# Kernel tuning notes

Measured on AMD Instinct MI355X. Metric: run time of the kernel, lower is better.

Reference implementation:

```python
import jax, jax.numpy as jnp
import numpy as np

B, T, D, H = 4, 2048, 1024, 16
HD = D // H  # head_dim = 64

def setup_inputs() -> dict:
    key = jax.random.key(0)
    k1, k2, k3 = jax.random.split(key, 3)
    scale_in = 1.0 / np.sqrt(D)
    return {
        "x": jax.random.normal(k1, (B, T, D), dtype=jnp.float32),
        "W_qkv": jax.random.normal(k2, (D, 3 * D), dtype=jnp.float32) * scale_in,
        "b_qkv": jnp.zeros((3 * D,), dtype=jnp.float32),
        "W_out": jax.random.normal(k3, (D, D), dtype=jnp.float32) * scale_in,
        "b_out": jnp.zeros((D,), dtype=jnp.float32),
    }

def reference(x, W_qkv, b_qkv, W_out, b_out):
    Bx, Tx, C = x.shape
    qkv = x @ W_qkv + b_qkv                      # [B,T,3D]
    q, k, v = jnp.split(qkv, 3, axis=-1)
    # [B,T,D] -> [B,H,T,hd]
    def to_heads(t):
        return t.reshape(Bx, Tx, H, HD).transpose(0, 2, 1, 3)
    q, k, v = to_heads(q), to_heads(k), to_heads(v)
    scores = jnp.einsum('bhqd,bhkd->bhqk', q, k) / np.sqrt(HD)  # [B,H,T,T]
    causal = jnp.tril(jnp.ones((Tx, Tx), dtype=bool))
    scores = jnp.where(causal, scores, -jnp.inf)
    attn = jax.nn.softmax(scores, axis=-1)       # dropout p=0 -> identity
    out = jnp.einsum('bhqk,bhkd->bhqd', attn, v)  # [B,H,T,hd]
    out = out.transpose(0, 2, 1, 3).reshape(Bx, Tx, C)
    return out @ W_out + b_out
```

## Files before the change

### kernel.cpp

```cpp
#include <hip/hip_runtime.h>
#include <hip/hip_bf16.h>

#define BB 4
#define TT 2048
#define DD 1024
#define HH 16
#define HDIM 64
#define BT (BB*TT)
#define D3 (3*DD)

typedef __attribute__((ext_vector_type(8))) short bf16x8;
typedef __attribute__((ext_vector_type(4))) float f32x4;

#if __has_builtin(__builtin_amdgcn_exp2f)
#define EXP2(x) __builtin_amdgcn_exp2f(x)
#else
#define EXP2(x) exp2f(x)
#endif

__device__ __forceinline__ ushort f2bf(float f) {
  union { float f; uint32_t u; } v; v.f = f;
  uint32_t u = v.u + 0x7FFFu + ((v.u >> 16) & 1u);
  return (ushort)(u >> 16);
}

__device__ __forceinline__ ushort f2bf_hw(float f) {
  __hip_bfloat16 h = __float2bfloat16(f);
  ushort u;
  __builtin_memcpy(&u, &h, 2);
  return u;
}

__device__ __forceinline__ float bf2f(ushort u) {
  union { uint32_t i; float f; } x; x.i = ((uint32_t)u) << 16; return x.f;
}

__device__ __forceinline__ void gload_lds16(const void* g, void* l) {
  __builtin_amdgcn_global_load_lds((const __attribute__((address_space(1))) void*)g,
                                   (__attribute__((address_space(3))) void*)l, 16, 0, 0);
}

__global__ __launch_bounds__(256)
void cvt_bf16(const float* __restrict__ in, ushort* __restrict__ out, int n4,
              uint* __restrict__ ctr) {
  if (blockIdx.x == 0 && threadIdx.x == 0) *ctr = 0u;
  int i = blockIdx.x * blockDim.x + threadIdx.x;
  int stride = gridDim.x * blockDim.x;
  for (; i < n4; i += stride) {
    float4 v = ((const float4*)in)[i];
    ushort4 o;
    o.x = f2bf(v.x); o.y = f2bf(v.y); o.z = f2bf(v.z); o.w = f2bf(v.w);
    ((ushort4*)out)[i] = o;
  }
}

__global__ __launch_bounds__(256)
void transpose_cvt(const float* __restrict__ W, ushort* __restrict__ Wt, int K, int N) {
  __shared__ ushort Tt[64][68];
  const int n0 = blockIdx.x * 64;
  const int k0 = blockIdx.y * 64;
  const int tid = threadIdx.x;
  const int r = tid >> 4;
  const int c4 = (tid & 15) * 4;
  #pragma unroll
  for (int i = 0; i < 4; ++i) {
    int row = r + i * 16;
    float4 v = *(const float4*)&W[(size_t)(k0 + row) * N + n0 + c4];
    Tt[c4 + 0][row] = f2bf(v.x);
    Tt[c4 + 1][row] = f2bf(v.y);
    Tt[c4 + 2][row] = f2bf(v.z);
    Tt[c4 + 3][row] = f2bf(v.w);
  }
  __syncthreads();
  #pragma unroll
  for (int i = 0; i < 4; ++i) {
    int row = r + i * 16;
    ushort4 tv = *(const ushort4*)&Tt[row][c4];
    *(ushort4*)&Wt[(size_t)(n0 + row) * K + k0 + c4] = tv;
  }
}

template<bool F32OUT>
__global__ __launch_bounds__(512, 2)
void gemm_8p(const ushort* __restrict__ A, const ushort* __restrict__ Bw,
             const float* __restrict__ bias, void* __restrict__ C, int N) {
  __shared__ __align__(16) short lds[2 * (128 + 256) * 64];

  const int tid = threadIdx.x;
  const int w = tid >> 6;
  const int wm = w >> 2;
  const int wn = w & 3;
  const int lane = tid & 63;
  const int li = lane & 15, g = lane >> 4;
  const int swz = (li & 7) << 4;

  const int bm = blockIdx.y * 128;
  const int bn = blockIdx.x * 256;
  const ushort* Ag = A + (size_t)bm * 1024;
  const ushort* Bg = Bw + (size_t)bn * 1024;

  const int lrow8 = lane >> 3;
  const int chsw = (lane & 7) ^ lrow8;

  f32x4 acc[4][4] = {};

#define STAGE6(t, p) do { \
  const int kk_ = (t) * 64; \
  short* Ad_ = lds + (p) * 24576; \
  short* Bd_ = Ad_ + 8192; \
  _Pragma("unroll") \
  for (int h_ = 0; h_ < 2; ++h_) { \
    const int r_ = h_ * 64 + w * 8; \
    gload_lds16(Ag + (size_t)(r_ + lrow8) * 1024 + kk_ + chsw * 8, Ad_ + r_ * 64); \
  } \
  _Pragma("unroll") \
  for (int j_ = 0; j_ < 4; ++j_) { \
    const int r_ = j_ * 64 + w * 8; \
    gload_lds16(Bg + (size_t)(r_ + lrow8) * 1024 + kk_ + chsw * 8, Bd_ + r_ * 64); \
  } \
} while (0)

  STAGE6(0, 0);
  asm volatile("s_waitcnt vmcnt(0)" ::: "memory");
  __builtin_amdgcn_sched_barrier(0);
  __builtin_amdgcn_s_barrier();

  for (int s = 0; s < 16; ++s) {
    const int cur = s & 1;
    const char* Ab = (const char*)lds + cur * 49152;
    const char* Bb = Ab + 16384;

    if (s + 1 < 16) STAGE6(s + 1, cur ^ 1);

    #pragma unroll
    for (int kh = 0; kh < 2; ++kh) {
      bf16x8 af[4], bf[4];
      #pragma unroll
      for (int mi = 0; mi < 4; ++mi)
        af[mi] = *(const bf16x8*)(Ab + (wm * 64 + mi * 16 + li) * 128 + ((kh * 64 + g * 16) ^ swz));
      #pragma unroll
      for (int ni = 0; ni < 4; ++ni)
        bf[ni] = *(const bf16x8*)(Bb + (wn * 64 + ni * 16 + li) * 128 + ((kh * 64 + g * 16) ^ swz));
      __builtin_amdgcn_s_setprio(1);
      #pragma unroll
      for (int mi = 0; mi < 4; ++mi)
        #pragma unroll
        for (int ni = 0; ni < 4; ++ni)
          acc[mi][ni] = __builtin_amdgcn_mfma_f32_16x16x32_bf16(af[mi], bf[ni], acc[mi][ni], 0, 0, 0);
      __builtin_amdgcn_s_setprio(0);
      if (kh == 0) __builtin_amdgcn_s_barrier();
    }
    asm volatile("s_waitcnt vmcnt(0)" ::: "memory");
    __builtin_amdgcn_sched_barrier(0);
    __builtin_amdgcn_s_barrier();
  }
#undef STAGE6

  #pragma unroll
  for (int ni = 0; ni < 4; ++ni) {
    int col = bn + wn * 64 + ni * 16 + li;
    float bv = bias[col];
    #pragma unroll
    for (int mi = 0; mi < 4; ++mi) {
      int row = bm + wm * 64 + mi * 16 + g * 4;
      #pragma unroll
      for (int r = 0; r < 4; ++r) {
        float v = acc[mi][ni][r] + bv;
        if (F32OUT) ((float*)C)[(size_t)(row + r) * N + col] = v;
        else        ((ushort*)C)[(size_t)(row + r) * N + col] = f2bf_hw(v);
      }
    }
  }
}

#define NITEMS 1024

__global__ __launch_bounds__(256)
void attn_mfma(const ushort* __restrict__ qkv, ushort* __restrict__ out,
               uint* __restrict__ ctr) {
  __shared__ __align__(16) short Ks[64 * 64];
  __shared__ __align__(16) short Vt[64 * 64];
  __shared__ __align__(16) short Pl[4 * 16 * 64];
  __shared__ int s_item;

  const int tid = threadIdx.x;
  const int w = tid >> 6;
  const int lane = tid & 63;
  const int li = lane & 15, g = lane >> 4;
  const int sw = (li & 7) << 4;

  char* KsB = (char*)Ks;
  char* VtB = (char*)Vt;
  char* PlB = (char*)Pl + w * 2048;

  const int krow0 = tid >> 3;
  const int kc = tid & 7;
  const int d0 = (tid >> 5) * 8;
  const int kp = tid & 31;
  const int kswz = (kc * 16) ^ ((krow0 & 7) << 4);

  for (;;) {
    if (tid == 0) s_item = (int)atomicAdd(ctr, 1u);
    __syncthreads();
    const int item = s_item;
    if (item >= NITEMS) return;

    const int qt = 15 - (item >> 6);
    const int bh = item & 63;
    const int h = bh & 15, b = bh >> 4;
    const int qg0 = qt * 128 + w * 32;

    bf16x8 qfr[2][2];
    #pragma unroll
    for (int qf = 0; qf < 2; ++qf) {
      const ushort* qrow = qkv + (size_t)(b * TT + qg0 + qf * 16 + li) * D3 + h * HDIM;
      #pragma unroll
      for (int c = 0; c < 2; ++c) {
        uint4 raw = *(const uint4*)(qrow + c * 32 + g * 8);
        const ushort* rp = (const ushort*)&raw;
        bf16x8 v;
        #pragma unroll
        for (int j = 0; j < 8; ++j)
          v[j] = (short)f2bf_hw(bf2f(rp[j]) * 0.18033688f);
        qfr[qf][c] = v;
      }
    }

    f32x4 o[4][2] = {};
    float lsum[2] = {0.f, 0.f};

    const ushort* kbase = qkv + (size_t)b * TT * D3 + DD + h * HDIM;
    const ushort* vbase = kbase + DD;

    const int nt = 2 * qt + 2;
    const int itlast = 2 * qt + (w >> 1);

    uint4 kpre0, kpre1, vpre0, vpre1;
    {
      const ushort* kg = kbase + (size_t)krow0 * D3 + kc * 8;
      kpre0 = *(const uint4*)kg;
      kpre1 = *(const uint4*)(kg + (size_t)32 * D3);
      const ushort* vg = vbase + (size_t)(2 * kp) * D3 + d0;
      vpre0 = *(const uint4*)vg;
      vpre1 = *(const uint4*)(vg + D3);
    }

    for (int it = 0; it < nt; ++it) {
      const int k0 = it * 64;
      *(uint4*)(KsB + krow0 * 128 + kswz) = kpre0;
      *(uint4*)(KsB + (krow0 + 32) * 128 + kswz) = kpre1;
      {
        const ushort* pa = (const ushort*)&vpre0;
        const ushort* pb = (const ushort*)&vpre1;
        #pragma unroll
        for (int j = 0; j < 8; ++j) {
          uint32_t pk = (uint32_t)pa[j] | ((uint32_t)pb[j] << 16);
          *(uint32_t*)(VtB + (d0 + j) * 128 + ((4 * kp) ^ (j << 4))) = pk;
        }
      }
      __syncthreads();
      if (it + 1 < nt) {
        const ushort* kg = kbase + (size_t)(k0 + 64 + krow0) * D3 + kc * 8;
        kpre0 = *(const uint4*)kg;
        kpre1 = *(const uint4*)(kg + (size_t)32 * D3);
        const ushort* vg = vbase + (size_t)(k0 + 64 + 2 * kp) * D3 + d0;
        vpre0 = *(const uint4*)vg;
        vpre1 = *(const uint4*)(vg + D3);
      }
      if (it <= itlast) {
        const bool domask = (it == itlast);
        bf16x8 pf[2][2];
        f32x4 s[2][4];
        __builtin_amdgcn_s_setprio(1);
        #pragma unroll
        for (int kt = 0; kt < 4; ++kt) {
          const int row = kt * 16 + li;
          bf16x8 kf0 = *(bf16x8*)(KsB + row * 128 + ((g * 16) ^ sw));
          bf16x8 kf1 = *(bf16x8*)(KsB + row * 128 + ((64 + g * 16) ^ sw));
          #pragma unroll
          for (int qf = 0; qf < 2; ++qf) {
            f32x4 a = {0.f, 0.f, 0.f, 0.f};
            a = __builtin_amdgcn_mfma_f32_16x16x32_bf16(kf0, qfr[qf][0], a, 0, 0, 0);
            a = __builtin_amdgcn_mfma_f32_16x16x32_bf16(kf1, qfr[qf][1], a, 0, 0, 0);
            s[qf][kt] = a;
          }
        }
        __builtin_amdgcn_s_setprio(0);
        #pragma unroll
        for (int qf = 0; qf < 2; ++qf) {
          const int qrow = qg0 + qf * 16 + li;
          if (domask) {
            #pragma unroll
            for (int kt = 0; kt < 4; ++kt)
              #pragma unroll
              for (int r = 0; r < 4; ++r) {
                int key = k0 + kt * 16 + g * 4 + r;
                if (key > qrow) s[qf][kt][r] = -1e30f;
              }
          }
          float ls = 0.f;
          #pragma unroll
          for (int kt = 0; kt < 4; ++kt) {
            float p0 = EXP2(s[qf][kt][0]);
            float p1 = EXP2(s[qf][kt][1]);
            float p2 = EXP2(s[qf][kt][2]);
            float p3 = EXP2(s[qf][kt][3]);
            ls += (p0 + p1) + (p2 + p3);
            uint2 val;
            val.x = (uint32_t)f2bf_hw(p0) | ((uint32_t)f2bf_hw(p1) << 16);
            val.y = (uint32_t)f2bf_hw(p2) | ((uint32_t)f2bf_hw(p3) << 16);
            *(uint2*)(PlB + li * 128 + ((kt * 32 + g * 8) ^ sw)) = val;
          }
          lsum[qf] += ls;
          pf[qf][0] = *(bf16x8*)(PlB + li * 128 + ((g * 16) ^ sw));
          pf[qf][1] = *(bf16x8*)(PlB + li * 128 + ((64 + g * 16) ^ sw));
        }
        __builtin_amdgcn_s_setprio(1);
        #pragma unroll
        for (int dt = 0; dt < 4; ++dt) {
          const int vrow = dt * 16 + li;
          bf16x8 vf0 = *(bf16x8*)(VtB + vrow * 128 + ((g * 16) ^ sw));
          bf16x8 vf1 = *(bf16x8*)(VtB + vrow * 128 + ((64 + g * 16) ^ sw));
          #pragma unroll
          for (int qf = 0; qf < 2; ++qf) {
            o[dt][qf] = __builtin_amdgcn_mfma_f32_16x16x32_bf16(vf0, pf[qf][0], o[dt][qf], 0, 0, 0);
            o[dt][qf] = __builtin_amdgcn_mfma_f32_16x16x32_bf16(vf1, pf[qf][1], o[dt][qf], 0, 0, 0);
          }
        }
        __builtin_amdgcn_s_setprio(0);
      }
      __syncthreads();
    }

    #pragma unroll
    for (int qf = 0; qf < 2; ++qf) {
      float lt = lsum[qf];
      lt += __shfl_xor(lt, 16);
      lt += __shfl_xor(lt, 32);
      float inv = 1.f / lt;
      ushort* orow = out + (size_t)(b * TT + qg0 + qf * 16 + li) * DD + h * HDIM;
      #pragma unroll
      for (int dt = 0; dt < 4; ++dt) {
        uint2 pk;
        pk.x = (uint32_t)f2bf_hw(o[dt][qf][0] * inv) | ((uint32_t)f2bf_hw(o[dt][qf][1] * inv) << 16);
        pk.y = (uint32_t)f2bf_hw(o[dt][qf][2] * inv) | ((uint32_t)f2bf_hw(o[dt][qf][3] * inv) << 16);
        *(uint2*)&orow[dt * 16 + g * 4] = pk;
      }
    }
  }
}

extern "C" void kernel_launch(void* const* d_in, const int* in_sizes, int n_in,
                              void* d_out, int out_size, void* d_ws, size_t ws_size,
                              hipStream_t stream) {
  const float* x     = (const float*)d_in[0];
  const float* W_qkv = (const float*)d_in[1];
  const float* b_qkv = (const float*)d_in[2];
  const float* W_out = (const float*)d_in[3];
  const float* b_out = (const float*)d_in[4];
  float* out = (float*)d_out;

  ushort* x_bf   = (ushort*)d_ws;
  ushort* wtq    = x_bf + (size_t)BT * DD;
  ushort* wto    = wtq + (size_t)D3 * DD;
  ushort* qkv_bf = wto + (size_t)DD * DD;
  ushort* att_bf = qkv_bf + (size_t)BT * D3;
  uint*   ctr    = (uint*)(att_bf + (size_t)BT * DD);

  cvt_bf16<<<2048, 256, 0, stream>>>(x, x_bf, BT * DD / 4, ctr);
  transpose_cvt<<<dim3(D3 / 64, DD / 64), 256, 0, stream>>>(W_qkv, wtq, DD, D3);
  transpose_cvt<<<dim3(DD / 64, DD / 64), 256, 0, stream>>>(W_out, wto, DD, DD);

  gemm_8p<false><<<dim3(D3 / 256, BT / 128), 512, 0, stream>>>(x_bf, wtq, b_qkv, (void*)qkv_bf, D3);
  attn_mfma<<<dim3(1280), 256, 0, stream>>>(qkv_bf, att_bf, ctr);
  gemm_8p<true><<<dim3(DD / 256, BT / 128), 512, 0, stream>>>(att_bf, wto, b_out, (void*)out, DD);
}
```

Baseline: 183.8 us.

## Double the attention KV tile to 128 keys per barrier iteration

The attention kernel now stages 128 keys of K and V into shared memory per loop iteration and processes them as two 64-key sub-tiles, halving the number of __syncthreads barriers and prefetch rounds. V is transposed into a wider 256-byte-row layout with an adjusted swizzle, and four rows per thread are prefetched instead of two. The grid shrinks from 1280 to 1024 persistent blocks. The cost is more LDS and registers per block, which may lower occupancy, and wasted load work on the final half-tile for odd tile counts.

Result: slower. 197.7 us (+7.6%).

```diff
diff --git a/kernel.cpp b/kernel.cpp
--- a/kernel.cpp
+++ b/kernel.cpp
@@ -178,8 +178,8 @@
 __global__ __launch_bounds__(256)
 void attn_mfma(const ushort* __restrict__ qkv, ushort* __restrict__ out,
                uint* __restrict__ ctr) {
-  __shared__ __align__(16) short Ks[64 * 64];
-  __shared__ __align__(16) short Vt[64 * 64];
+  __shared__ __align__(16) short Ks[128 * 64];
+  __shared__ __align__(16) short Vt[64 * 128];
   __shared__ __align__(16) short Pl[4 * 16 * 64];
   __shared__ int s_item;
 
@@ -232,102 +232,115 @@
     const ushort* kbase = qkv + (size_t)b * TT * D3 + DD + h * HDIM;
     const ushort* vbase = kbase + DD;
 
-    const int nt = 2 * qt + 2;
+    const int nIter = qt + 1;
     const int itlast = 2 * qt + (w >> 1);
 
-    uint4 kpre0, kpre1, vpre0, vpre1;
+    uint4 kpre[4], vpre[4];
     {
       const ushort* kg = kbase + (size_t)krow0 * D3 + kc * 8;
-      kpre0 = *(const uint4*)kg;
-      kpre1 = *(const uint4*)(kg + (size_t)32 * D3);
-      const ushort* vg = vbase + (size_t)(2 * kp) * D3 + d0;
-      vpre0 = *(const uint4*)vg;
-      vpre1 = *(const uint4*)(vg + D3);
-    }
-
-    for (int it = 0; it < nt; ++it) {
-      const int k0 = it * 64;
-      *(uint4*)(KsB + krow0 * 128 + kswz) = kpre0;
-      *(uint4*)(KsB + (krow0 + 32) * 128 + kswz) = kpre1;
+      #pragma unroll
+      for (int i = 0; i < 4; ++i)
+        kpre[i] = *(const uint4*)(kg + (size_t)(32 * i) * D3);
+      const ushort* vg = vbase + (size_t)(4 * kp) * D3 + d0;
+      #pragma unroll
+      for (int j = 0; j < 4; ++j)
+        vpre[j] = *(const uint4*)(vg + (size_t)j * D3);
+    }
+
+    for (int it = 0; it < nIter; ++it) {
+      #pragma unroll
+      for (int i = 0; i < 4; ++i)
+        *(uint4*)(KsB + (krow0 + 32 * i) * 128 + kswz) = kpre[i];
       {
-        const ushort* pa = (const ushort*)&vpre0;
-        const ushort* pb = (const ushort*)&vpre1;
+        const ushort* p0 = (const ushort*)&vpre[0];
+        const ushort* p1 = (const ushort*)&vpre[1];
+        const ushort* p2 = (const ushort*)&vpre[2];
+        const ushort* p3 = (const ushort*)&vpre[3];
         #pragma unroll
         for (int j = 0; j < 8; ++j) {
-          uint32_t pk = (uint32_t)pa[j] | ((uint32_t)pb[j] << 16);
-          *(uint32_t*)(VtB + (d0 + j) * 128 + ((4 * kp) ^ (j << 4))) = pk;
+          uint32_t lo = (uint32_t)p0[j] | ((uint32_t)p1[j] << 16);
+          uint32_t hi = (uint32_t)p2[j] | ((uint32_t)p3[j] << 16);
+          *(uint32_t*)(VtB + (d0 + j) * 256 + ((8 * kp) ^ (j << 4))) = lo;
+          *(uint32_t*)(VtB + (d0 + j) * 256 + ((8 * kp + 4) ^ (j << 4))) = hi;
         }
       }
       __syncthreads();
-      if (it + 1 < nt) {
-        const ushort* kg = kbase + (size_t)(k0 + 64 + krow0) * D3 + kc * 8;
-        kpre0 = *(const uint4*)kg;
-        kpre1 = *(const uint4*)(kg + (size_t)32 * D3);
-        const ushort* vg = vbase + (size_t)(k0 + 64 + 2 * kp) * D3 + d0;
-        vpre0 = *(const uint4*)vg;
-        vpre1 = *(const uint4*)(vg + D3);
-      }
-      if (it <= itlast) {
-        const bool domask = (it == itlast);
-        bf16x8 pf[2][2];
-        f32x4 s[2][4];
-        __builtin_amdgcn_s_setprio(1);
-        #pragma unroll
-        for (int kt = 0; kt < 4; ++kt) {
-          const int row = kt * 16 + li;
-          bf16x8 kf0 = *(bf16x8*)(KsB + row * 128 + ((g * 16) ^ sw));
-          bf16x8 kf1 = *(bf16x8*)(KsB + row * 128 + ((64 + g * 16) ^ sw));
+      if (it + 1 < nIter) {
+        const ushort* kg = kbase + (size_t)((it + 1) * 128 + krow0) * D3 + kc * 8;
+        #pragma unroll
+        for (int i = 0; i < 4; ++i)
+          kpre[i] = *(const uint4*)(kg + (size_t)(32 * i) * D3);
+        const ushort* vg = vbase + (size_t)((it + 1) * 128 + 4 * kp) * D3 + d0;
+        #pragma unroll
+        for (int j = 0; j < 4; ++j)
+          vpre[j] = *(const uint4*)(vg + (size_t)j * D3);
+      }
+      #pragma unroll
+      for (int c = 0; c < 2; ++c) {
+        const int t = 2 * it + c;
+        if (t <= itlast) {
+          const bool domask = (t == itlast);
+          const int k0 = t * 64;
+          bf16x8 pf[2][2];
+          f32x4 s[2][4];
+          __builtin_amdgcn_s_setprio(1);
+          #pragma unroll
+          for (int kt = 0; kt < 4; ++kt) {
+            const int row = c * 64 + kt * 16 + li;
+            bf16x8 kf0 = *(bf16x8*)(KsB + row * 128 + ((g * 16) ^ sw));
+            bf16x8 kf1 = *(bf16x8*)(KsB + row * 128 + ((64 + g * 16) ^ sw));
+            #pragma unroll
+            for (int qf = 0; qf < 2; ++qf) {
+              f32x4 a = {0.f, 0.f, 0.f, 0.f};
+              a = __builtin_amdgcn_mfma_f32_16x16x32_bf16(kf0, qfr[qf][0], a, 0, 0, 0);
+              a = __builtin_amdgcn_mfma_f32_16x16x32_bf16(kf1, qfr[qf][1], a, 0, 0, 0);
+              s[qf][kt] = a;
+            }
+          }
+          __builtin_amdgcn_s_setprio(0);
           #pragma unroll
           for (int qf = 0; qf < 2; ++qf) {
-            f32x4 a = {0.f, 0.f, 0.f, 0.f};
-            a = __builtin_amdgcn_mfma_f32_16x16x32_bf16(kf0, qfr[qf][0], a, 0, 0, 0);
-            a = __builtin_amdgcn_mfma_f32_16x16x32_bf16(kf1, qfr[qf][1], a, 0, 0, 0);
-            s[qf][kt] = a;
+            const int qrow = qg0 + qf * 16 + li;
+            if (domask) {
+              #pragma unroll
+              for (int kt = 0; kt < 4; ++kt)
+                #pragma unroll
+                for (int r = 0; r < 4; ++r) {
+                  int key = k0 + kt * 16 + g * 4 + r;
+                  if (key > qrow) s[qf][kt][r] = -1e30f;
+                }
+            }
+            float ls = 0.f;
+            #pragma unroll
+            for (int kt = 0; kt < 4; ++kt) {
+              float p0 = EXP2(s[qf][kt][0]);
+              float p1 = EXP2(s[qf][kt][1]);
+              float p2 = EXP2(s[qf][kt][2]);
+              float p3 = EXP2(s[qf][kt][3]);
+              ls += (p0 + p1) + (p2 + p3);
+              uint2 val;
+              val.x = (uint32_t)f2bf_hw(p0) | ((uint32_t)f2bf_hw(p1) << 16);
+              val.y = (uint32_t)f2bf_hw(p2) | ((uint32_t)f2bf_hw(p3) << 16);
+              *(uint2*)(PlB + li * 128 + ((kt * 32 + g * 8) ^ sw)) = val;
+            }
+            lsum[qf] += ls;
+            pf[qf][0] = *(bf16x8*)(PlB + li * 128 + ((g * 16) ^ sw));
+            pf[qf][1] = *(bf16x8*)(PlB + li * 128 + ((64 + g * 16) ^ sw));
           }
+          __builtin_amdgcn_s_setprio(1);
+          #pragma unroll
+          for (int dt = 0; dt < 4; ++dt) {
+            const int vrow = dt * 16 + li;
+            bf16x8 vf0 = *(bf16x8*)(VtB + vrow * 256 + ((c * 128 + g * 16) ^ sw));
+            bf16x8 vf1 = *(bf16x8*)(VtB + vrow * 256 + ((c * 128 + 64 + g * 16) ^ sw));
+            #pragma unroll
+            for (int qf = 0; qf < 2; ++qf) {
+              o[dt][qf] = __builtin_amdgcn_mfma_f32_16x16x32_bf16(vf0, pf[qf][0], o[dt][qf], 0, 0, 0);
+              o[dt][qf] = __builtin_amdgcn_mfma_f32_16x16x32_bf16(vf1, pf[qf][1], o[dt][qf], 0, 0, 0);
+            }
+          }
+          __builtin_amdgcn_s_setprio(0);
         }
-        __builtin_amdgcn_s_setprio(0);
-        #pragma unroll
-        for (int qf = 0; qf < 2; ++qf) {
-          const int qrow = qg0 + qf * 16 + li;
-          if (domask) {
-            #pragma unroll
-            for (int kt = 0; kt < 4; ++kt)
-              #pragma unroll
-              for (int r = 0; r < 4; ++r) {
-                int key = k0 + kt * 16 + g * 4 + r;
-                if (key > qrow) s[qf][kt][r] = -1e30f;
-              }
-          }
-          float ls = 0.f;
-          #pragma unroll
-          for (int kt = 0; kt < 4; ++kt) {
-            float p0 = EXP2(s[qf][kt][0]);
-            float p1 = EXP2(s[qf][kt][1]);
-            float p2 = EXP2(s[qf][kt][2]);
-            float p3 = EXP2(s[qf][kt][3]);
-            ls += (p0 + p1) + (p2 + p3);
-            uint2 val;
-            val.x = (uint32_t)f2bf_hw(p0) | ((uint32_t)f2bf_hw(p1) << 16);
-            val.y = (uint32_t)f2bf_hw(p2) | ((uint32_t)f2bf_hw(p3) << 16);
-            *(uint2*)(PlB + li * 128 + ((kt * 32 + g * 8) ^ sw)) = val;
-          }
-          lsum[qf] += ls;
-          pf[qf][0] = *(bf16x8*)(PlB + li * 128 + ((g * 16) ^ sw));
-          pf[qf][1] = *(bf16x8*)(PlB + li * 128 + ((64 + g * 16) ^ sw));
-        }
-        __builtin_amdgcn_s_setprio(1);
-        #pragma unroll
-        for (int dt = 0; dt < 4; ++dt) {
-          const int vrow = dt * 16 + li;
-          bf16x8 vf0 = *(bf16x8*)(VtB + vrow * 128 + ((g * 16) ^ sw));
-          bf16x8 vf1 = *(bf16x8*)(VtB + vrow * 128 + ((64 + g * 16) ^ sw));
-          #pragma unroll
-          for (int qf = 0; qf < 2; ++qf) {
-            o[dt][qf] = __builtin_amdgcn_mfma_f32_16x16x32_bf16(vf0, pf[qf][0], o[dt][qf], 0, 0, 0);
-            o[dt][qf] = __builtin_amdgcn_mfma_f32_16x16x32_bf16(vf1, pf[qf][1], o[dt][qf], 0, 0, 0);
-          }
-        }
-        __builtin_amdgcn_s_setprio(0);
       }
       __syncthreads();
     }
@@ -372,6 +385,6 @@
   transpose_cvt<<<dim3(DD / 64, DD / 64), 256, 0, stream>>>(W_out, wto, DD, DD);
 
   gemm_8p<false><<<dim3(D3 / 256, BT / 128), 512, 0, stream>>>(x_bf, wtq, b_qkv, (void*)qkv_bf, D3);
-  attn_mfma<<<dim3(1280), 256, 0, stream>>>(qkv_bf, att_bf, ctr);
+  attn_mfma<<<dim3(1024), 256, 0, stream>>>(qkv_bf, att_bf, ctr);
   gemm_8p<true><<<dim3(DD / 256, BT / 128), 512, 0, stream>>>(att_bf, wto, b_out, (void*)out, DD);
 }
```
